# Performance work log

Measured on AMD Instinct MI355X. Metric: run time of the kernel, lower is better.

## Reference

```python
import jax, jax.numpy as jnp
import numpy as np

BS, C, T = 8, 4096, 512          # batch, channels/tokens, flattened spatial (= q_dim)
H, HD = 8, 64                     # n_heads, head_dim = output_dim // n_heads
OUT_DIM = 512
SCALE = float(np.sqrt(OUT_DIM))   # module uses sqrt(output_dim), not sqrt(head_dim)


def setup_inputs() -> dict:
    key = jax.random.key(0)
    ks = jax.random.split(key, 7)
    init = 0.02
    return {
        "q": jax.random.normal(ks[0], (BS, C, T), jnp.float32),
        "k": jax.random.normal(ks[1], (BS, C, T), jnp.float32),
        "v": jax.random.normal(ks[2], (BS, C, T), jnp.float32),
        # per-head Linear weights, torch layout (out, in) stacked over heads
        "Wq": jax.random.normal(ks[3], (H, HD, T), jnp.float32) * init,
        "Wk": jax.random.normal(ks[4], (H, HD, T), jnp.float32) * init,
        "Wv": jax.random.normal(ks[5], (H, HD, T), jnp.float32) * init,
        "Wo": jax.random.normal(ks[6], (OUT_DIM, H * HD), jnp.float32) * init,
    }


def reference(q, k, v, Wq, Wk, Wv, Wo):
    bs, c, t = q.shape
    # batched per-head projections: (b, C, T) x (H, HD, T) -> (b, H, C, HD)
    qh = jnp.einsum("bct,hdt->bhcd", q, Wq)
    kh = jnp.einsum("bct,hdt->bhcd", k, Wk)
    vh = jnp.einsum("bct,hdt->bhcd", v, Wv)
    # attention contracts over the channel axis c (faithful to 'bct,bcs->bts')
    scores = jnp.einsum("bhcd,bhce->bhde", qh, kh) / SCALE  # (b, H, HD, HD)
    w = jax.nn.softmax(scores, axis=-1)
    # 'bts,bcs->bct' per head -> (b, H, C, HD)
    attn = jnp.einsum("bhde,bhce->bhcd", w, vh)
    # concat heads along last dim: (b, C, H*HD)
    cat = attn.transpose(0, 2, 1, 3).reshape(bs, c, H * HD)
    out = cat @ Wo.T  # (b, C, OUT_DIM); dropout p=0 -> identity
    return out.reshape(bs, -1, t)  # view(bs, -1, *spatial)
```

## Files before the change

kernel.cpp:

```cpp
#include <hip/hip_runtime.h>

#define BS    8
#define CDIM  4096
#define TDIM  512
#define NH    8
#define HD    64
#define NDIM  512
#define INV_SCALE 0.044194173824159216f

typedef __bf16 bf16x8 __attribute__((ext_vector_type(8)));
typedef float  f32x4  __attribute__((ext_vector_type(4)));

static __device__ __forceinline__ unsigned short f2b(float f) {
    union { float f; unsigned int i; } x; x.f = f;
    unsigned int r = x.i + 0x7FFFu + ((x.i >> 16) & 1u);
    return (unsigned short)(r >> 16);
}

static __device__ __forceinline__ void gl2lds16(const unsigned short* g,
                                                unsigned short* l) {
    __builtin_amdgcn_global_load_lds(
        (const __attribute__((address_space(1))) void*)g,
        (__attribute__((address_space(3))) void*)l, 16, 0, 0);
}

__global__ __launch_bounds__(256) void transpose_qk_kernel(
    const float* __restrict__ q, const float* __restrict__ k,
    unsigned short* __restrict__ qT, unsigned short* __restrict__ kT)
{
    __shared__ unsigned int Ls[64 * 33];

    const int z = blockIdx.z;
    const int b = z & 7;
    const float* src = (z >> 3) ? k : q;
    unsigned short* dst = (z >> 3) ? kT : qT;

    const int c0 = blockIdx.x * 64;
    const int t0 = blockIdx.y * 64;
    const int tid = threadIdx.x;

    {
        const int cp = tid >> 3, seg = (tid & 7) * 8;
        const float* p0 = src + ((size_t)b * CDIM + c0 + 2 * cp) * TDIM + t0 + seg;
        const float* p1 = p0 + TDIM;
        float4 a0 = *(const float4*)p0, a1 = *(const float4*)(p0 + 4);
        float4 b0 = *(const float4*)p1, b1 = *(const float4*)(p1 + 4);
        float r0[8] = {a0.x, a0.y, a0.z, a0.w, a1.x, a1.y, a1.z, a1.w};
        float r1[8] = {b0.x, b0.y, b0.z, b0.w, b1.x, b1.y, b1.z, b1.w};
#pragma unroll
        for (int j = 0; j < 8; j++)
            Ls[(seg + j) * 33 + cp] =
                (unsigned int)f2b(r0[j]) | ((unsigned int)f2b(r1[j]) << 16);
    }
    __syncthreads();
    {
        const int tp = tid >> 2, cs = (tid & 3) * 8;
        alignas(16) unsigned int u[8];
#pragma unroll
        for (int j = 0; j < 8; j++) u[j] = Ls[tp * 33 + cs + j];
        unsigned short* o = dst + ((size_t)b * TDIM + t0 + tp) * CDIM + c0 + cs * 2;
        *(uint4*)o       = *(const uint4*)&u[0];
        *(uint4*)(o + 8) = *(const uint4*)&u[4];
    }
}

__global__ __launch_bounds__(256) void cvt_kernel(
    const float* __restrict__ in, unsigned short* __restrict__ out, int n8)
{
    int i = blockIdx.x * 256 + threadIdx.x;
    if (i >= n8) return;
    float4 f0 = ((const float4*)in)[i * 2], f1 = ((const float4*)in)[i * 2 + 1];
    alignas(16) unsigned short t[8] = {f2b(f0.x), f2b(f0.y), f2b(f0.z), f2b(f0.w),
                                       f2b(f1.x), f2b(f1.y), f2b(f1.z), f2b(f1.w)};
    ((float4*)out)[i] = *(const float4*)t;
}

__global__ __launch_bounds__(256) void gemm128_kernel(
    const unsigned short* __restrict__ A, size_t sAb,
    const unsigned short* __restrict__ B, size_t sBb,
    void* __restrict__ Cv, int c_f32, int writeT, int ldc, size_t sCb,
    int ldk, int K, int zshift, int zmask, size_t sCsplit)
{
    __shared__ unsigned short As[5][128 * 32];
    __shared__ unsigned short Bs[5][128 * 32];

    const int tid  = threadIdx.x;
    const int wave = tid >> 6, lane = tid & 63;
    const int quad = lane >> 4, l16 = lane & 15;
    const int wm = wave >> 1, wn = wave & 1;
    const int m0 = blockIdx.x * 128, n0 = blockIdx.y * 128;
    const int z = blockIdx.z;
    const int b = z >> zshift, ks = z & zmask;
    const int kbase = ks * K;

    const unsigned short* Ab = A + (size_t)b * sAb;
    const unsigned short* Bb = B + (size_t)b * sBb;

    f32x4 acc[4][4];
#pragma unroll
    for (int i = 0; i < 4; i++)
#pragma unroll
        for (int j = 0; j < 4; j++) acc[i][j] = (f32x4){0.f, 0.f, 0.f, 0.f};

    const int ldr  = lane >> 2;
    const int fr_w = (ldr & 3) ^ ((ldr >> 2) & 1);
    const int gcol = ((lane & 3) ^ fr_w) * 8;
    const int fr_r = (l16 & 3) ^ ((l16 >> 2) & 1);
    const int qsw  = (quad ^ fr_r) * 8;

    const int nt = K / 32;

    auto stage = [&](int t) {
        const int kk = kbase + t * 32;
        unsigned short* as = &As[t % 5][0];
        unsigned short* bs = &Bs[t % 5][0];
#pragma unroll
        for (int i = 0; i < 2; i++) {
            const int panel = wave * 2 + i;
            gl2lds16(&Ab[(size_t)(m0 + panel * 16 + ldr) * ldk + kk + gcol],
                     &as[panel * 512]);
            gl2lds16(&Bb[(size_t)(n0 + panel * 16 + ldr) * ldk + kk + gcol],
                     &bs[panel * 512]);
        }
    };

    stage(0);
    if (nt > 1) stage(1);
    if (nt > 2) stage(2);

    for (int t = 0; t < nt; ++t) {
        if (t + 3 < nt) stage(t + 3);
        const int ahead = nt - 1 - t;
        if (ahead >= 3)      asm volatile("s_waitcnt vmcnt(12)" ::: "memory");
        else if (ahead == 2) asm volatile("s_waitcnt vmcnt(8)"  ::: "memory");
        else if (ahead == 1) asm volatile("s_waitcnt vmcnt(4)"  ::: "memory");
        else                 asm volatile("s_waitcnt vmcnt(0)"  ::: "memory");
        __builtin_amdgcn_s_barrier();
        asm volatile("" ::: "memory");

        const unsigned short* as = &As[t % 5][0];
        const unsigned short* bs = &Bs[t % 5][0];
        bf16x8 af[4], bf[4];
#pragma unroll
        for (int i = 0; i < 4; i++) {
            af[i] = *(const bf16x8*)&as[(wm * 64 + i * 16 + l16) * 32 + qsw];
            bf[i] = *(const bf16x8*)&bs[(wn * 64 + i * 16 + l16) * 32 + qsw];
        }
#pragma unroll
        for (int mb = 0; mb < 4; mb++)
#pragma unroll
            for (int nb = 0; nb < 4; nb++)
                acc[mb][nb] = __builtin_amdgcn_mfma_f32_16x16x32_bf16(
                    af[mb], bf[nb], acc[mb][nb], 0, 0, 0);
    }

    const size_t offC = (size_t)b * sCb + (size_t)ks * sCsplit;
#pragma unroll
    for (int mb = 0; mb < 4; mb++)
#pragma unroll
        for (int nb = 0; nb < 4; nb++)
#pragma unroll
            for (int r = 0; r < 4; r++) {
                int row = m0 + wm * 64 + mb * 16 + quad * 4 + r;
                int col = n0 + wn * 64 + nb * 16 + l16;
                size_t idx = offC + (writeT ? (size_t)col * ldc + row
                                            : (size_t)row * ldc + col);
                if (c_f32) ((float*)Cv)[idx] = acc[mb][nb][r];
                else ((unsigned short*)Cv)[idx] = f2b(acc[mb][nb][r]);
            }
}

__global__ __launch_bounds__(256) void reduceG_kernel(
    const float* __restrict__ P, unsigned short* __restrict__ G)
{
    const int i = blockIdx.x * 256 + threadIdx.x;
    const float4* p = (const float4*)P + (size_t)i * 2;
    const size_t st = 2097152 / 4;
    float4 a0 = p[0], a1 = p[1];
#pragma unroll
    for (int s = 1; s < 4; s++) {
        float4 b0 = p[(size_t)s * st], b1 = p[(size_t)s * st + 1];
        a0.x += b0.x; a0.y += b0.y; a0.z += b0.z; a0.w += b0.w;
        a1.x += b1.x; a1.y += b1.y; a1.z += b1.z; a1.w += b1.w;
    }
    alignas(16) unsigned short t[8] = {f2b(a0.x), f2b(a0.y), f2b(a0.z), f2b(a0.w),
                                       f2b(a1.x), f2b(a1.y), f2b(a1.z), f2b(a1.w)};
    ((float4*)G)[i] = *(const float4*)t;
}

__global__ __launch_bounds__(256) void gemm64_kernel(
    const void* __restrict__ Av, int a_f32, size_t sAb, size_t sAh,
    const unsigned short* __restrict__ B, size_t sBb, size_t sBh,
    void* __restrict__ Cv, int c_f32, int writeT, int ldc, size_t sCb, size_t sCh,
    int K, int hshift, int hmask)
{
    __shared__ unsigned short As[64][40];
    __shared__ unsigned short Bs[64][40];

    const int tid  = threadIdx.x;
    const int wave = tid >> 6, lane = tid & 63;
    const int quad = lane >> 4, l16 = lane & 15;
    const int m0 = blockIdx.x * 64, n0 = blockIdx.y * 64;
    const int bz = blockIdx.z;
    const int b = bz >> hshift, h = bz & hmask;

    f32x4 acc[4];
#pragma unroll
    for (int i = 0; i < 4; i++) acc[i] = (f32x4){0.f, 0.f, 0.f, 0.f};

    const int ldrow = tid >> 2, ldseg = (tid & 3) * 8;
    const size_t offA = (size_t)b * sAb + (size_t)h * sAh;
    const size_t offB = (size_t)b * sBb + (size_t)h * sBh;

    for (int k0 = 0; k0 < K; k0 += 32) {
        __syncthreads();
        if (a_f32) {
            const float* p = (const float*)Av + offA + (size_t)(m0 + ldrow) * K + k0 + ldseg;
            float4 lo = *(const float4*)p, hi = *(const float4*)(p + 4);
            alignas(16) unsigned short t8[8] = {
                f2b(lo.x), f2b(lo.y), f2b(lo.z), f2b(lo.w),
                f2b(hi.x), f2b(hi.y), f2b(hi.z), f2b(hi.w)};
            *(float4*)&As[ldrow][ldseg] = *(const float4*)t8;
        } else {
            const unsigned short* p = (const unsigned short*)Av + offA +
                                      (size_t)(m0 + ldrow) * K + k0 + ldseg;
            *(float4*)&As[ldrow][ldseg] = *(const float4*)p;
        }
        {
            const unsigned short* p = B + offB + (size_t)(n0 + ldrow) * K + k0 + ldseg;
            *(float4*)&Bs[ldrow][ldseg] = *(const float4*)p;
        }
        __syncthreads();

        bf16x8 a = *(const bf16x8*)&As[wave * 16 + l16][quad * 8];
#pragma unroll
        for (int nb = 0; nb < 4; nb++) {
            bf16x8 bb = *(const bf16x8*)&Bs[nb * 16 + l16][quad * 8];
            acc[nb] = __builtin_amdgcn_mfma_f32_16x16x32_bf16(a, bb, acc[nb], 0, 0, 0);
        }
    }

    const size_t offC = (size_t)b * sCb + (size_t)h * sCh;
#pragma unroll
    for (int nb = 0; nb < 4; nb++)
#pragma unroll
        for (int r = 0; r < 4; r++) {
            int row = m0 + wave * 16 + quad * 4 + r;
            int col = n0 + nb * 16 + l16;
            size_t idx = offC + (writeT ? (size_t)col * ldc + row
                                        : (size_t)row * ldc + col);
            if (c_f32) ((float*)Cv)[idx] = acc[nb][r];
            else ((unsigned short*)Cv)[idx] = f2b(acc[nb][r]);
        }
}

__global__ __launch_bounds__(256) void transpose_wv_kernel(
    const float* __restrict__ Wv, unsigned short* __restrict__ WvT)
{
    int i = blockIdx.x * 256 + threadIdx.x;
    int h = i >> 15, r = i & 32767;
    int t = r >> 6, e = i & 63;
    WvT[i] = f2b(Wv[(size_t)h * 32768 + (size_t)e * 512 + t]);
}

__global__ __launch_bounds__(64) void softmax_kernel(
    const float* __restrict__ S, unsigned short* __restrict__ w)
{
    const int bh = blockIdx.x;
    const int d  = threadIdx.x;
    const float* s = S + (size_t)bh * (HD * HD) + d * HD;
    float v[64];
    float m = -1e30f;
#pragma unroll
    for (int e = 0; e < 64; e++) { v[e] = s[e] * INV_SCALE; m = fmaxf(m, v[e]); }
    float sum = 0.f;
#pragma unroll
    for (int e = 0; e < 64; e++) { v[e] = __expf(v[e] - m); sum += v[e]; }
    float rinv = 1.0f / sum;
    unsigned short* o = w + (size_t)bh * (HD * HD) + d * HD;
#pragma unroll
    for (int e = 0; e < 64; e++) o[e] = f2b(v[e] * rinv);
}

extern "C" void kernel_launch(void* const* d_in, const int* in_sizes, int n_in,
                              void* d_out, int out_size, void* d_ws, size_t ws_size,
                              hipStream_t stream)
{
    const float* q  = (const float*)d_in[0];
    const float* k  = (const float*)d_in[1];
    const float* v  = (const float*)d_in[2];
    const float* Wq = (const float*)d_in[3];
    const float* Wk = (const float*)d_in[4];
    const float* Wv = (const float*)d_in[5];
    const float* Wo = (const float*)d_in[6];

    unsigned short* qT   = (unsigned short*)d_ws;
    unsigned short* kT   = qT + 16777216;
    unsigned short* G    = kT + 16777216;
    unsigned short* tmpT = G + 2097152;
    unsigned short* WkB  = tmpT + 2097152;
    unsigned short* WoB  = WkB + 262144;
    unsigned short* WvT  = WoB + 262144;
    unsigned short* w    = WvT + 262144;
    unsigned short* WveT = w + 262144;
    unsigned short* W2   = WveT + 2097152;
    float*          S    = (float*)(W2 + 2097152);
    float*          P1   = (float*)tmpT;
    unsigned short* vB   = qT;

    transpose_qk_kernel<<<dim3(64, 8, 16), 256, 0, stream>>>(q, k, qT, kT);

    gemm128_kernel<<<dim3(4, 4, BS * 4), 256, 0, stream>>>(
        qT, 2097152, kT, 2097152,
        P1, 1, 0, 512, 262144, 4096, 1024, 2, 3, 2097152);

    cvt_kernel<<<8192, 256, 0, stream>>>(v, vB, 2097152);

    reduceG_kernel<<<1024, 256, 0, stream>>>(P1, G);

    cvt_kernel<<<128, 256, 0, stream>>>(Wk, WkB, 32768);
    cvt_kernel<<<128, 256, 0, stream>>>(Wo, WoB, 32768);
    transpose_wv_kernel<<<1024, 256, 0, stream>>>(Wv, WvT);

    gemm64_kernel<<<dim3(8, 8, 8), 256, 0, stream>>>(
        G, 0, 262144, 0, WkB, 0, 0,
        tmpT, 0, 1, 512, 262144, 0, 512, 0, 0);

    gemm64_kernel<<<dim3(1, 1, 64), 256, 0, stream>>>(
        Wq, 1, 0, 32768, tmpT, 262144, 32768,
        S, 1, 0, 64, 32768, 4096, 512, 3, 7);

    softmax_kernel<<<64, 64, 0, stream>>>(S, w);

    gemm64_kernel<<<dim3(1, 8, 64), 256, 0, stream>>>(
        w, 0, 32768, 4096, WvT, 0, 32768,
        WveT, 0, 1, 512, 262144, 64, 64, 3, 7);

    gemm64_kernel<<<dim3(8, 8, 8), 256, 0, stream>>>(
        WoB, 0, 0, 0, WveT, 262144, 0,
        W2, 0, 0, 512, 262144, 0, 512, 0, 0);

    gemm128_kernel<<<dim3(32, 4, BS), 256, 0, stream>>>(
        vB, 2097152, W2, 262144,
        d_out, 1, 0, 512, 2097152, 512, 512, 0, 0, 0);
}
```

Baseline: 367.0 us.

## Fuse q/k bf16 transpose into the Q^T K gemm reading fp32 directly

Removes the separate transpose_qk kernel that wrote bf16 transposed copies of q and k, and replaces the first gemm with a new kernel that loads fp32 q and k, converts to bf16 in registers and stores them into swizzled LDS in transposed form. It uses a register-prefetched, double-buffered LDS pipeline feeding bf16 MFMAs with a 4-way split over the channel axis. This removes a full write and re-read of 2x32 MB of bf16 intermediates. In exchange the gemm reads twice the bytes (fp32) and does the conversion work inline, with shallower buffering than the old 5-stage gemm.

```diff
diff --git a/kernel.cpp b/kernel.cpp
--- a/kernel.cpp
+++ b/kernel.cpp
@@ -24,45 +24,11 @@
         (__attribute__((address_space(3))) void*)l, 16, 0, 0);
 }
 
-__global__ __launch_bounds__(256) void transpose_qk_kernel(
-    const float* __restrict__ q, const float* __restrict__ k,
-    unsigned short* __restrict__ qT, unsigned short* __restrict__ kT)
-{
-    __shared__ unsigned int Ls[64 * 33];
-
-    const int z = blockIdx.z;
-    const int b = z & 7;
-    const float* src = (z >> 3) ? k : q;
-    unsigned short* dst = (z >> 3) ? kT : qT;
-
-    const int c0 = blockIdx.x * 64;
-    const int t0 = blockIdx.y * 64;
-    const int tid = threadIdx.x;
-
-    {
-        const int cp = tid >> 3, seg = (tid & 7) * 8;
-        const float* p0 = src + ((size_t)b * CDIM + c0 + 2 * cp) * TDIM + t0 + seg;
-        const float* p1 = p0 + TDIM;
-        float4 a0 = *(const float4*)p0, a1 = *(const float4*)(p0 + 4);
-        float4 b0 = *(const float4*)p1, b1 = *(const float4*)(p1 + 4);
-        float r0[8] = {a0.x, a0.y, a0.z, a0.w, a1.x, a1.y, a1.z, a1.w};
-        float r1[8] = {b0.x, b0.y, b0.z, b0.w, b1.x, b1.y, b1.z, b1.w};
-#pragma unroll
-        for (int j = 0; j < 8; j++)
-            Ls[(seg + j) * 33 + cp] =
-                (unsigned int)f2b(r0[j]) | ((unsigned int)f2b(r1[j]) << 16);
-    }
-    __syncthreads();
-    {
-        const int tp = tid >> 2, cs = (tid & 3) * 8;
-        alignas(16) unsigned int u[8];
-#pragma unroll
-        for (int j = 0; j < 8; j++) u[j] = Ls[tp * 33 + cs + j];
-        unsigned short* o = dst + ((size_t)b * TDIM + t0 + tp) * CDIM + c0 + cs * 2;
-        *(uint4*)o       = *(const uint4*)&u[0];
-        *(uint4*)(o + 8) = *(const uint4*)&u[4];
-    }
-}
+#define LDS_BARRIER() do {                                           \
+    asm volatile("s_waitcnt lgkmcnt(0)" ::: "memory");               \
+    __builtin_amdgcn_s_barrier();                                    \
+    asm volatile("" ::: "memory");                                   \
+} while (0)
 
 __global__ __launch_bounds__(256) void cvt_kernel(
     const float* __restrict__ in, unsigned short* __restrict__ out, int n8)
@@ -73,6 +39,119 @@
     alignas(16) unsigned short t[8] = {f2b(f0.x), f2b(f0.y), f2b(f0.z), f2b(f0.w),
                                        f2b(f1.x), f2b(f1.y), f2b(f1.z), f2b(f1.w)};
     ((float4*)out)[i] = *(const float4*)t;
+}
+
+__global__ __launch_bounds__(256) void gemmTN128_kernel(
+    const float* __restrict__ Q, const float* __restrict__ Kf,
+    float* __restrict__ P)
+{
+    __shared__ unsigned int As[2][128 * 16];
+    __shared__ unsigned int Bs[2][128 * 16];
+
+    const int tid  = threadIdx.x;
+    const int wave = tid >> 6, lane = tid & 63;
+    const int quad = lane >> 4, l16 = lane & 15;
+    const int wm = wave >> 1, wn = wave & 1;
+    const int m0 = blockIdx.x * 128, n0 = blockIdx.y * 128;
+    const int z = blockIdx.z;
+    const int b = z >> 2, ks = z & 3;
+    const int kbase = ks * 1024;
+
+    const float* Qb = Q + (size_t)b * (CDIM * TDIM);
+    const float* Kb = Kf + (size_t)b * (CDIM * TDIM);
+
+    const int cp = tid >> 4;
+    const int ts = (tid & 15) * 8;
+
+    f32x4 acc[4][4];
+#pragma unroll
+    for (int i = 0; i < 4; i++)
+#pragma unroll
+        for (int j = 0; j < 4; j++) acc[i][j] = (f32x4){0.f, 0.f, 0.f, 0.f};
+
+    float4 qA0, qA1, qA2, qA3, kA0, kA1, kA2, kA3;
+    float4 qB0, qB1, qB2, qB3, kB0, kB1, kB2, kB3;
+
+#define ISSUE(TK, QR, KR) do {                                           \
+    const int c0_ = kbase + (TK) * 32 + 2 * cp;                          \
+    const float* q_ = Qb + (size_t)c0_ * TDIM + m0 + ts;                 \
+    const float* k_ = Kb + (size_t)c0_ * TDIM + n0 + ts;                 \
+    QR##0 = *(const float4*)q_;           QR##1 = *(const float4*)(q_ + 4); \
+    QR##2 = *(const float4*)(q_ + TDIM);  QR##3 = *(const float4*)(q_ + TDIM + 4); \
+    KR##0 = *(const float4*)k_;           KR##1 = *(const float4*)(k_ + 4); \
+    KR##2 = *(const float4*)(k_ + TDIM);  KR##3 = *(const float4*)(k_ + TDIM + 4); \
+} while (0)
+
+#define STORE8(DST, X0, X1, X2, X3) do {                                 \
+    const float lo_[8] = {X0.x, X0.y, X0.z, X0.w, X1.x, X1.y, X1.z, X1.w}; \
+    const float hi_[8] = {X2.x, X2.y, X2.z, X2.w, X3.x, X3.y, X3.z, X3.w}; \
+    _Pragma("unroll")                                                    \
+    for (int j_ = 0; j_ < 8; j_++) {                                     \
+        const int m_ = ts + j_;                                          \
+        const int ch_ = ((cp >> 2) ^ (m_ >> 3)) & 3;                     \
+        (DST)[m_ * 16 + ch_ * 4 + (cp & 3)] =                            \
+            (unsigned int)f2b(lo_[j_]) |                                 \
+            ((unsigned int)f2b(hi_[j_]) << 16);                          \
+    }                                                                    \
+} while (0)
+
+#define COMPUTE(BUF) do {                                                \
+    bf16x8 af[4], bf[4];                                                 \
+    _Pragma("unroll")                                                    \
+    for (int i_ = 0; i_ < 4; i_++) {                                     \
+        const int ma_ = wm * 64 + i_ * 16 + l16;                         \
+        const int ca_ = (quad ^ (ma_ >> 3)) & 3;                         \
+        af[i_] = *(const bf16x8*)&As[BUF][ma_ * 16 + ca_ * 4];           \
+        const int mb_ = wn * 64 + i_ * 16 + l16;                         \
+        const int cb_ = (quad ^ (mb_ >> 3)) & 3;                         \
+        bf[i_] = *(const bf16x8*)&Bs[BUF][mb_ * 16 + cb_ * 4];           \
+    }                                                                    \
+    _Pragma("unroll")                                                    \
+    for (int mb2 = 0; mb2 < 4; mb2++)                                    \
+        _Pragma("unroll")                                                \
+        for (int nb2 = 0; nb2 < 4; nb2++)                                \
+            acc[mb2][nb2] = __builtin_amdgcn_mfma_f32_16x16x32_bf16(     \
+                af[mb2], bf[nb2], acc[mb2][nb2], 0, 0, 0);               \
+} while (0)
+
+    const int nt = 32;
+
+    ISSUE(0, qA, kA);
+    ISSUE(1, qB, kB);
+    STORE8(As[0], qA0, qA1, qA2, qA3);
+    STORE8(Bs[0], kA0, kA1, kA2, kA3);
+    LDS_BARRIER();
+
+    for (int t = 0; t < nt; t += 2) {
+        if (t + 2 < nt) ISSUE(t + 2, qA, kA);
+        COMPUTE(0);
+        STORE8(As[1], qB0, qB1, qB2, qB3);
+        STORE8(Bs[1], kB0, kB1, kB2, kB3);
+        LDS_BARRIER();
+        if (t + 3 < nt) ISSUE(t + 3, qB, kB);
+        COMPUTE(1);
+        if (t + 2 < nt) {
+            STORE8(As[0], qA0, qA1, qA2, qA3);
+            STORE8(Bs[0], kA0, kA1, kA2, kA3);
+        }
+        LDS_BARRIER();
+    }
+
+#undef ISSUE
+#undef STORE8
+#undef COMPUTE
+
+    float* Pb = P + (size_t)ks * 2097152 + (size_t)b * 262144;
+#pragma unroll
+    for (int mb = 0; mb < 4; mb++)
+#pragma unroll
+        for (int nb = 0; nb < 4; nb++)
+#pragma unroll
+            for (int r = 0; r < 4; r++) {
+                int row = m0 + wm * 64 + mb * 16 + quad * 4 + r;
+                int col = n0 + wn * 64 + nb * 16 + l16;
+                Pb[(size_t)row * 512 + col] = acc[mb][nb][r];
+            }
 }
 
 __global__ __launch_bounds__(256) void gemm128_kernel(
@@ -308,11 +387,7 @@
     float*          P1   = (float*)tmpT;
     unsigned short* vB   = qT;
 
-    transpose_qk_kernel<<<dim3(64, 8, 16), 256, 0, stream>>>(q, k, qT, kT);
-
-    gemm128_kernel<<<dim3(4, 4, BS * 4), 256, 0, stream>>>(
-        qT, 2097152, kT, 2097152,
-        P1, 1, 0, 512, 262144, 4096, 1024, 2, 3, 2097152);
+    gemmTN128_kernel<<<dim3(4, 4, BS * 4), 256, 0, stream>>>(q, k, P1);
 
     cvt_kernel<<<8192, 256, 0, stream>>>(v, vB, 2097152);
 
```

New measurement: 354.2 us. -3.5%, faster.
